# Kernel tuning notes

Hardware: AMD Instinct MI355X
Metric: run time of the kernel (lower is better)

## Reference

```python
import jax, jax.numpy as jnp
import numpy as np

N_NODES = 100000
N_EDGES = 1600000
N_GRAPHS = 1000
D = 128
LATENT = 64
N_LAYERS = 3
EPS = 1e-5


def leaky(z):
    return jnp.where(z >= 0, z, 0.2 * z)


def batchnorm(h, gamma, beta):
    # training-mode BN: biased batch statistics over axis 0
    m = jnp.mean(h, axis=0)
    v = jnp.mean(jnp.square(h - m), axis=0)
    return (h - m) * jax.lax.rsqrt(v + EPS) * gamma + beta


def setup_inputs() -> dict:
    key = jax.random.key(0)
    ks = jax.random.split(key, 8)
    x = jax.random.normal(ks[0], (N_NODES, D), dtype=jnp.float32)
    edge_index = jax.random.randint(ks[1], (2, N_EDGES), 0, N_NODES, dtype=jnp.int32)
    batch = jnp.sort(jax.random.randint(ks[2], (N_NODES,), 0, N_GRAPHS, dtype=jnp.int32))
    s = 1.0 / np.sqrt(D)
    W1 = jax.random.normal(ks[3], (N_LAYERS, D, D), dtype=jnp.float32) * s
    W2 = jax.random.normal(ks[4], (N_LAYERS, D, D), dtype=jnp.float32) * s
    fc_W = jax.random.normal(ks[5], (D, LATENT), dtype=jnp.float32) * s
    return {
        'x': x, 'edge_index': edge_index, 'batch': batch,
        'W1': W1, 'b1': jnp.zeros((N_LAYERS, D), jnp.float32),
        'g1': jnp.ones((N_LAYERS, D), jnp.float32), 'bt1': jnp.zeros((N_LAYERS, D), jnp.float32),
        'W2': W2, 'b2': jnp.zeros((N_LAYERS, D), jnp.float32),
        'bn_g': jnp.ones((D,), jnp.float32), 'bn_b': jnp.zeros((D,), jnp.float32),
        'fc_W': fc_W, 'fc_b': jnp.zeros((LATENT,), jnp.float32),
    }


def reference(x, edge_index, batch, W1, b1, g1, bt1, W2, b2, bn_g, bn_b, fc_W, fc_b):
    src, dst = edge_index[0], edge_index[1]
    n = x.shape[0]
    for l in range(N_LAYERS):
        x_res = x
        # GIN aggregation: (1 + eps) * x + sum_{j in N(i)} x_j, eps = 0
        agg = jax.ops.segment_sum(x[src], dst, num_segments=n) + x
        h = leaky(agg @ W1[l] + b1[l])
        h = batchnorm(h, g1[l], bt1[l])
        h = leaky(h @ W2[l] + b2[l])
        x = h + x_res  # residual (dropout disabled in eval)
    pooled = jax.ops.segment_sum(x, batch, num_segments=N_GRAPHS)  # [G, D]
    out = batchnorm(pooled, bn_g, bn_b)
    return out @ fc_W + fc_b
```

## Files before the change

kernel.cpp:

```cpp
#include <hip/hip_runtime.h>

#define N_NODES 100000
#define N_EDGES 1600000
#define N_GRAPHS 1000
#define D 128
#define LATENT 64
#define EPS 1e-5f
#define NB ((N_NODES + 255) / 256)
#define NBUCK 196
#define BSH 9
#define CONVX_BLOCKS ((N_NODES * D / 4 + 255) / 256)

typedef unsigned short u16;
typedef unsigned int u32;
typedef __attribute__((ext_vector_type(8))) short short8;
typedef __attribute__((ext_vector_type(4))) float f32x4;

__device__ __forceinline__ float bf2f(u32 u) {
    union { u32 i; float f; } c; c.i = u << 16; return c.f;
}
__device__ __forceinline__ u16 f2bf(float f) {
    union { float f; u32 u; } c; c.f = f;
    u32 u = c.u;
    return (u16)((u + 0x7fffu + ((u >> 16) & 1u)) >> 16);
}


__global__ void init_misc(const float* __restrict__ W1, const float* __restrict__ W2,
                          u16* __restrict__ Wt, const float* __restrict__ x,
                          u16* __restrict__ xb, float* __restrict__ colsumAll,
                          int* __restrict__ bhist,
                          int* __restrict__ gs, int* __restrict__ ge) {
    int b = blockIdx.x, t = threadIdx.x;
    if (b < 6) {
        const float* src = (b < 3) ? (W1 + (size_t)b * D * D) : (W2 + (size_t)(b - 3) * D * D);
        u16* dst = Wt + (size_t)b * D * D;
        for (int i = t; i < D * D; i += 256) {
            int k = i >> 7, n = i & 127;
            dst[n * D + k] = f2bf(src[i]);
        }
    } else if (b == 6) {
        for (int i = t; i < 6 * 256; i += 256) colsumAll[i] = 0.f;
        if (t < NBUCK) bhist[t] = 0;
        for (int i = t; i < N_GRAPHS; i += 256) { gs[i] = 0x7fffffff; ge[i] = 0; }
    } else {
        int idx = (b - 7) * 256 + t;
        if (idx < N_NODES * D / 4) {
            float4 v = *(const float4*)&x[(size_t)idx * 4];
            u32 lo = (u32)f2bf(v.x) | ((u32)f2bf(v.y) << 16);
            u32 hi = (u32)f2bf(v.z) | ((u32)f2bf(v.w) << 16);
            *(uint2*)&xb[(size_t)idx * 4] = make_uint2(lo, hi);
        }
    }
}


__global__ void bucket_hist(const int* __restrict__ dst, int* __restrict__ bhist) {
    __shared__ int cnt[256];
    int t = threadIdx.x;
    cnt[t] = 0;
    __syncthreads();
    int base = blockIdx.x * 4096 + t * 16;
#pragma unroll
    for (int i = 0; i < 16; ++i) {
        int e = base + i;
        if (e < N_EDGES) atomicAdd(&cnt[dst[e] >> BSH], 1);
    }
    __syncthreads();
    if (t < NBUCK && cnt[t] > 0) atomicAdd(&bhist[t], cnt[t]);
}

__global__ void bucket_scan(const int* __restrict__ bhist, int* __restrict__ bstart,
                            int* __restrict__ gbcur) {
    __shared__ int s[256];
    int t = threadIdx.x;
    int v = (t < NBUCK) ? bhist[t] : 0;
    s[t] = v;
    __syncthreads();
    for (int off = 1; off < 256; off <<= 1) {
        int a = (t >= off) ? s[t - off] : 0;
        __syncthreads();
        s[t] += a;
        __syncthreads();
    }
    if (t < NBUCK) { int ex = s[t] - v; bstart[t] = ex; gbcur[t] = ex; }
    if (t == NBUCK - 1) bstart[NBUCK] = s[t];
}

__global__ __launch_bounds__(256)
void bucket_scatter(const int* __restrict__ src, const int* __restrict__ dst,
                    int* __restrict__ gbcur, u32* __restrict__ ebp) {
    __shared__ int cnt[256], loff[256], basev[256], scn[256];
    __shared__ u32 pp[4096];
    __shared__ unsigned char pbkt[4096];
    int t = threadIdx.x;
    cnt[t] = 0;
    __syncthreads();
    int ebase = blockIdx.x * 4096;
    int b[16], r[16];
    u32 pk[16];
#pragma unroll
    for (int i = 0; i < 16; ++i) {
        int e = ebase + t * 16 + i;
        bool ok = e < N_EDGES;
        int d = ok ? dst[e] : 0;
        int sv = ok ? src[e] : 0;
        pk[i] = ((u32)sv << BSH) | (u32)(d & 511);
        b[i] = ok ? (d >> BSH) : -1;
    }
#pragma unroll
    for (int i = 0; i < 16; ++i)
        r[i] = (b[i] >= 0) ? atomicAdd(&cnt[b[i]], 1) : 0;
    __syncthreads();
    int c = cnt[t];
    scn[t] = c;
    __syncthreads();
    for (int off = 1; off < 256; off <<= 1) {
        int a = (t >= off) ? scn[t - off] : 0;
        __syncthreads();
        scn[t] += a;
        __syncthreads();
    }
    loff[t] = scn[t] - c;
    if (c > 0) basev[t] = atomicAdd(&gbcur[t], c);
    __syncthreads();
#pragma unroll
    for (int i = 0; i < 16; ++i) {
        if (b[i] >= 0) {
            int p = loff[b[i]] + r[i];
            pp[p] = pk[i];
            pbkt[p] = (unsigned char)b[i];
        }
    }
    __syncthreads();
    int total = min(4096, N_EDGES - ebase);
    for (int i = t; i < total; i += 256) {
        int bb = pbkt[i];
        int g = basev[bb] + (i - loff[bb]);
        ebp[g] = pp[i];
    }
}

__global__ void hist_local(const u32* __restrict__ ebp, const int* __restrict__ bstart,
                           int* __restrict__ deg) {
    __shared__ int h[512];
    int b = blockIdx.x, t = threadIdx.x;
    int nbase = b << BSH;
    h[t] = 0; h[t + 256] = 0;
    __syncthreads();
    int e0 = bstart[b], e1 = bstart[b + 1];
    for (int e = e0 + t; e < e1; e += 256)
        atomicAdd(&h[ebp[e] & 511], 1);
    __syncthreads();
    int nlen = min(512, N_NODES - nbase);
    if (t < nlen) deg[nbase + t] = h[t];
    if (t + 256 < nlen) deg[nbase + t + 256] = h[t + 256];
}

__global__ void scan_block_sum(const int* __restrict__ deg, int* __restrict__ bsum) {
    __shared__ int s[256];
    int t = threadIdx.x;
    int i = blockIdx.x * 256 + t;
    s[t] = (i < N_NODES) ? deg[i] : 0;
    __syncthreads();
    for (int off = 128; off > 0; off >>= 1) {
        if (t < off) s[t] += s[t + off];
        __syncthreads();
    }
    if (t == 0) bsum[blockIdx.x] = s[0];
}

__global__ void scan_top(const int* __restrict__ bsum, int* __restrict__ boff) {
    __shared__ int s[512];
    int t = threadIdx.x;
    int v = (t < NB) ? bsum[t] : 0;
    s[t] = v;
    __syncthreads();
    for (int off = 1; off < 512; off <<= 1) {
        int add = (t >= off) ? s[t - off] : 0;
        __syncthreads();
        s[t] += add;
        __syncthreads();
    }
    if (t < NB) boff[t] = s[t] - v;
}

__global__ void scan_apply(const int* __restrict__ deg, const int* __restrict__ boff,
                           int* __restrict__ offsets) {
    __shared__ int s[256];
    int t = threadIdx.x;
    int i = blockIdx.x * 256 + t;
    int v = (i < N_NODES) ? deg[i] : 0;
    s[t] = v;
    __syncthreads();
    for (int off = 1; off < 256; off <<= 1) {
        int add = (t >= off) ? s[t - off] : 0;
        __syncthreads();
        s[t] += add;
        __syncthreads();
    }
    int base = boff[blockIdx.x];
    if (i < N_NODES) offsets[i] = base + s[t] - v;
    if (i == N_NODES - 1) offsets[N_NODES] = base + s[t];
}

__global__ void csr_fill_local(const u32* __restrict__ ebp, const int* __restrict__ bstart,
                               const int* __restrict__ offsets, int* __restrict__ csr) {
    __shared__ int cur[512];
    int b = blockIdx.x, t = threadIdx.x;
    int nbase = b << BSH;
    int nlen = min(512, N_NODES - nbase);
    if (t < nlen) cur[t] = offsets[nbase + t];
    if (t + 256 < nlen) cur[t + 256] = offsets[nbase + t + 256];
    __syncthreads();
    int e0 = bstart[b], e1 = bstart[b + 1];
    for (int e = e0 + t; e < e1; e += 256) {
        u32 pk = ebp[e];
        int p = atomicAdd(&cur[pk & 511], 1);
        csr[p] = (int)(pk >> BSH);
    }
}


__device__ __forceinline__ void acc8(float* a, uint4 v) {
    a[0] += bf2f(v.x & 0xffff); a[1] += bf2f(v.x >> 16);
    a[2] += bf2f(v.y & 0xffff); a[3] += bf2f(v.y >> 16);
    a[4] += bf2f(v.z & 0xffff); a[5] += bf2f(v.z >> 16);
    a[6] += bf2f(v.w & 0xffff); a[7] += bf2f(v.w >> 16);
}

__global__ void agg_kernel(const u16* __restrict__ xb, const int* __restrict__ csr,
                           const int* __restrict__ offsets, u16* __restrict__ ab) {
    int t = blockIdx.x * blockDim.x + threadIdx.x;
    int node = t >> 4;
    if (node >= N_NODES) return;
    int lane = t & 15;
    const uint4* xp = (const uint4*)(xb + lane * 8);
    float a[8] = {0, 0, 0, 0, 0, 0, 0, 0};
    acc8(a, xp[(size_t)node * 16]);
    int s = offsets[node], e = offsets[node + 1];
    int p = s;
    for (; p + 8 <= e; p += 8) {
        int j0 = csr[p], j1 = csr[p + 1], j2 = csr[p + 2], j3 = csr[p + 3];
        int j4 = csr[p + 4], j5 = csr[p + 5], j6 = csr[p + 6], j7 = csr[p + 7];
        uint4 v0 = xp[(size_t)j0 * 16];
        uint4 v1 = xp[(size_t)j1 * 16];
        uint4 v2 = xp[(size_t)j2 * 16];
        uint4 v3 = xp[(size_t)j3 * 16];
        uint4 v4 = xp[(size_t)j4 * 16];
        uint4 v5 = xp[(size_t)j5 * 16];
        uint4 v6 = xp[(size_t)j6 * 16];
        uint4 v7 = xp[(size_t)j7 * 16];
        acc8(a, v0); acc8(a, v1); acc8(a, v2); acc8(a, v3);
        acc8(a, v4); acc8(a, v5); acc8(a, v6); acc8(a, v7);
    }
    for (; p + 4 <= e; p += 4) {
        int j0 = csr[p], j1 = csr[p + 1], j2 = csr[p + 2], j3 = csr[p + 3];
        uint4 v0 = xp[(size_t)j0 * 16];
        uint4 v1 = xp[(size_t)j1 * 16];
        uint4 v2 = xp[(size_t)j2 * 16];
        uint4 v3 = xp[(size_t)j3 * 16];
        acc8(a, v0); acc8(a, v1); acc8(a, v2); acc8(a, v3);
    }
    for (; p < e; ++p)
        acc8(a, xp[(size_t)csr[p] * 16]);
    uint4 o;
    o.x = (u32)f2bf(a[0]) | ((u32)f2bf(a[1]) << 16);
    o.y = (u32)f2bf(a[2]) | ((u32)f2bf(a[3]) << 16);
    o.z = (u32)f2bf(a[4]) | ((u32)f2bf(a[5]) << 16);
    o.w = (u32)f2bf(a[6]) | ((u32)f2bf(a[7]) << 16);
    *(uint4*)&ab[(size_t)node * D + lane * 8] = o;
}


__global__ __launch_bounds__(256, 4)
void gemm1_mfma(u16* __restrict__ AB, const u16* __restrict__ Wt,
                const float* __restrict__ bias,
                float* __restrict__ colsum, float* __restrict__ colsq) {
    __shared__ u16 As[128 * 128];
    __shared__ float csumL[D], csqL[D];
    int tid = threadIdx.x;
    int row0 = blockIdx.x * 128;

    if (tid < D) { csumL[tid] = 0.f; csqL[tid] = 0.f; }
#pragma unroll
    for (int i = 0; i < 8; ++i) {
        int q = i * 256 + tid;
        int m = q >> 4, kc = q & 15;
        uint4 av = make_uint4(0, 0, 0, 0);
        int gm = row0 + m;
        if (gm < N_NODES) av = *(const uint4*)&AB[(size_t)gm * D + kc * 8];
        *(uint4*)((char*)As + m * 256 + ((kc * 16) ^ ((m & 15) << 4))) = av;
    }
    __syncthreads();

    int lane = tid & 63;
    int wid = tid >> 6;
    int mbase = (wid >> 1) * 64, nbase = (wid & 1) * 64;
    int lr = lane & 15, kg = lane >> 4;
    f32x4 acc[4][4];
#pragma unroll
    for (int mt = 0; mt < 4; ++mt)
#pragma unroll
        for (int nt = 0; nt < 4; ++nt) acc[mt][nt] = (f32x4)0.0f;

    const char* Ap = (const char*)As;
#pragma unroll
    for (int ks = 0; ks < 4; ++ks) {
        int kb2 = ks * 64 + kg * 16;
        short8 af[4], bfr[4];
#pragma unroll
        for (int t = 0; t < 4; ++t) {
            int m = mbase + t * 16 + lr;
            af[t] = *(const short8*)(Ap + m * 256 + (kb2 ^ ((m & 15) << 4)));
            int n = nbase + t * 16 + lr;
            bfr[t] = *(const short8*)&Wt[n * D + ks * 32 + kg * 8];
        }
#pragma unroll
        for (int mt = 0; mt < 4; ++mt)
#pragma unroll
            for (int nt = 0; nt < 4; ++nt)
                acc[mt][nt] = __builtin_amdgcn_mfma_f32_16x16x32_bf16(af[mt], bfr[nt], acc[mt][nt], 0, 0, 0);
    }

    float bv[4], ls[4] = {0, 0, 0, 0}, lq[4] = {0, 0, 0, 0};
#pragma unroll
    for (int nt = 0; nt < 4; ++nt) bv[nt] = bias[nbase + nt * 16 + lr];
#pragma unroll
    for (int mt = 0; mt < 4; ++mt) {
#pragma unroll
        for (int r = 0; r < 4; ++r) {
            int gm = row0 + mbase + mt * 16 + kg * 4 + r;
            if (gm < N_NODES) {
#pragma unroll
                for (int nt = 0; nt < 4; ++nt) {
                    float z = acc[mt][nt][r] + bv[nt];
                    z = (z >= 0.f) ? z : 0.2f * z;
                    AB[(size_t)gm * D + nbase + nt * 16 + lr] = f2bf(z);
                    ls[nt] += z; lq[nt] += z * z;
                }
            }
        }
    }
#pragma unroll
    for (int nt = 0; nt < 4; ++nt) {
        ls[nt] += __shfl_down(ls[nt], 32); ls[nt] += __shfl_down(ls[nt], 16);
        lq[nt] += __shfl_down(lq[nt], 32); lq[nt] += __shfl_down(lq[nt], 16);
    }
    if (lane < 16) {
#pragma unroll
        for (int nt = 0; nt < 4; ++nt) {
            atomicAdd(&csumL[nbase + nt * 16 + lane], ls[nt]);
            atomicAdd(&csqL[nbase + nt * 16 + lane], lq[nt]);
        }
    }
    __syncthreads();
    if (tid < D) {
        atomicAdd(&colsum[tid], csumL[tid]);
        atomicAdd(&colsq[tid], csqL[tid]);
    }
}

__global__ __launch_bounds__(256, 4)
void gemm2_mfma(const u16* __restrict__ HB, const u16* __restrict__ Wt,
                const float* __restrict__ bias,
                const float* __restrict__ colsum, const float* __restrict__ colsq,
                const float* __restrict__ gamma, const float* __restrict__ beta,
                const u16* __restrict__ xres, u16* __restrict__ xbout) {
    __shared__ u16 As[128 * 128];
    __shared__ float scL[D], shL[D];
    int tid = threadIdx.x;
    int row0 = blockIdx.x * 128;

    if (tid < D) {
        float m = colsum[tid] * (1.0f / N_NODES);
        float var = fmaxf(colsq[tid] * (1.0f / N_NODES) - m * m, 0.f);
        float sc = gamma[tid] * rsqrtf(var + EPS);
        scL[tid] = sc;
        shL[tid] = beta[tid] - m * sc;
    }
    __syncthreads();

#pragma unroll
    for (int i = 0; i < 8; ++i) {
        int q = i * 256 + tid;
        int m = q >> 4, kc = q & 15;
        uint4 av = make_uint4(0, 0, 0, 0);
        int gm = row0 + m;
        if (gm < N_NODES) {
            uint4 h = *(const uint4*)&HB[(size_t)gm * D + kc * 8];
            float4 s0 = *(const float4*)&scL[kc * 8];
            float4 s1 = *(const float4*)&scL[kc * 8 + 4];
            float4 t0 = *(const float4*)&shL[kc * 8];
            float4 t1 = *(const float4*)&shL[kc * 8 + 4];
            float f0 = bf2f(h.x & 0xffff) * s0.x + t0.x;
            float f1 = bf2f(h.x >> 16)    * s0.y + t0.y;
            float f2 = bf2f(h.y & 0xffff) * s0.z + t0.z;
            float f3 = bf2f(h.y >> 16)    * s0.w + t0.w;
            float f4 = bf2f(h.z & 0xffff) * s1.x + t1.x;
            float f5 = bf2f(h.z >> 16)    * s1.y + t1.y;
            float f6 = bf2f(h.w & 0xffff) * s1.z + t1.z;
            float f7 = bf2f(h.w >> 16)    * s1.w + t1.w;
            av.x = (u32)f2bf(f0) | ((u32)f2bf(f1) << 16);
            av.y = (u32)f2bf(f2) | ((u32)f2bf(f3) << 16);
            av.z = (u32)f2bf(f4) | ((u32)f2bf(f5) << 16);
            av.w = (u32)f2bf(f6) | ((u32)f2bf(f7) << 16);
        }
        *(uint4*)((char*)As + m * 256 + ((kc * 16) ^ ((m & 15) << 4))) = av;
    }
    __syncthreads();

    int lane = tid & 63;
    int wid = tid >> 6;
    int mbase = (wid >> 1) * 64, nbase = (wid & 1) * 64;
    int lr = lane & 15, kg = lane >> 4;
    f32x4 acc[4][4];
#pragma unroll
    for (int mt = 0; mt < 4; ++mt)
#pragma unroll
        for (int nt = 0; nt < 4; ++nt) acc[mt][nt] = (f32x4)0.0f;

    const char* Ap = (const char*)As;
#pragma unroll
    for (int ks = 0; ks < 4; ++ks) {
        int kb2 = ks * 64 + kg * 16;
        short8 af[4], bfr[4];
#pragma unroll
        for (int t = 0; t < 4; ++t) {
            int m = mbase + t * 16 + lr;
            af[t] = *(const short8*)(Ap + m * 256 + (kb2 ^ ((m & 15) << 4)));
            int n = nbase + t * 16 + lr;
            bfr[t] = *(const short8*)&Wt[n * D + ks * 32 + kg * 8];
        }
#pragma unroll
        for (int mt = 0; mt < 4; ++mt)
#pragma unroll
            for (int nt = 0; nt < 4; ++nt)
                acc[mt][nt] = __builtin_amdgcn_mfma_f32_16x16x32_bf16(af[mt], bfr[nt], acc[mt][nt], 0, 0, 0);
    }

    float bv[4];
#pragma unroll
    for (int nt = 0; nt < 4; ++nt) bv[nt] = bias[nbase + nt * 16 + lr];
#pragma unroll
    for (int mt = 0; mt < 4; ++mt) {
#pragma unroll
        for (int r = 0; r < 4; ++r) {
            int gm = row0 + mbase + mt * 16 + kg * 4 + r;
            if (gm < N_NODES) {
#pragma unroll
                for (int nt = 0; nt < 4; ++nt) {
                    int gn = nbase + nt * 16 + lr;
                    float z = acc[mt][nt][r] + bv[nt];
                    z = (z >= 0.f) ? z : 0.2f * z;
                    float o = z + bf2f((u32)xres[(size_t)gm * D + gn]);
                    xbout[(size_t)gm * D + gn] = f2bf(o);
                }
            }
        }
    }
}


__global__ void bounds_kernel(const int* __restrict__ batch, int* __restrict__ gs, int* __restrict__ ge) {
    int i = blockIdx.x * blockDim.x + threadIdx.x;
    if (i >= N_NODES) return;
    int b = batch[i];
    if (i == 0) {
        gs[b] = 0;
    } else {
        int bp = batch[i - 1];
        if (bp != b) { gs[b] = i; ge[bp] = i; }
    }
    if (i == N_NODES - 1) ge[b] = N_NODES;
}

__global__ void pool_kernel(const u16* __restrict__ xb, const int* __restrict__ gs,
                            const int* __restrict__ ge, float* __restrict__ pooled) {
    int g = blockIdx.x, f = threadIdx.x;
    int s = gs[g], e = ge[g];
    float a0 = 0.f, a1 = 0.f, a2 = 0.f, a3 = 0.f;
    int i = s;
    for (; i + 4 <= e; i += 4) {
        a0 += bf2f((u32)xb[(size_t)i * D + f]);
        a1 += bf2f((u32)xb[(size_t)(i + 1) * D + f]);
        a2 += bf2f((u32)xb[(size_t)(i + 2) * D + f]);
        a3 += bf2f((u32)xb[(size_t)(i + 3) * D + f]);
    }
    for (; i < e; ++i) a0 += bf2f((u32)xb[(size_t)i * D + f]);
    pooled[g * D + f] = (a0 + a1) + (a2 + a3);
}

__global__ void pooled_bn(const float* __restrict__ pooled, const float* __restrict__ g,
                          const float* __restrict__ b, float* __restrict__ pscale,
                          float* __restrict__ pshift) {
    int c = blockIdx.x;
    int t = threadIdx.x;
    float s = 0.f, q = 0.f;
    for (int gi = t; gi < N_GRAPHS; gi += 256) {
        float v = pooled[gi * D + c];
        s += v; q += v * v;
    }
#pragma unroll
    for (int off = 32; off > 0; off >>= 1) {
        s += __shfl_down(s, off);
        q += __shfl_down(q, off);
    }
    __shared__ float ss[4], qq[4];
    int lane = t & 63, w = t >> 6;
    if (lane == 0) { ss[w] = s; qq[w] = q; }
    __syncthreads();
    if (t == 0) {
        float S = (ss[0] + ss[1]) + (ss[2] + ss[3]);
        float Q = (qq[0] + qq[1]) + (qq[2] + qq[3]);
        float m = S / N_GRAPHS;
        float var = fmaxf(Q / N_GRAPHS - m * m, 0.f);
        float sc = g[c] * rsqrtf(var + EPS);
        pscale[c] = sc;
        pshift[c] = b[c] - m * sc;
    }
}

__global__ void out_kernel(const float* __restrict__ pooled, const float* __restrict__ pscale,
                           const float* __restrict__ pshift, const float* __restrict__ fcW,
                           const float* __restrict__ fcb, float* __restrict__ out) {
    int idx = blockIdx.x * blockDim.x + threadIdx.x;
    if (idx >= N_GRAPHS * LATENT) return;
    int g = idx >> 6, j = idx & 63;
    float acc = fcb[j];
    for (int c = 0; c < D; ++c) {
        float pv = pooled[g * D + c] * pscale[c] + pshift[c];
        acc += pv * fcW[c * LATENT + j];
    }
    out[idx] = acc;
}


extern "C" void kernel_launch(void* const* d_in, const int* in_sizes, int n_in,
                              void* d_out, int out_size, void* d_ws, size_t ws_size,
                              hipStream_t stream) {
    const float* x_in = (const float*)d_in[0];
    const int* edges  = (const int*)d_in[1];
    const int* batch  = (const int*)d_in[2];
    const float* W1   = (const float*)d_in[3];
    const float* b1   = (const float*)d_in[4];
    const float* g1   = (const float*)d_in[5];
    const float* bt1  = (const float*)d_in[6];
    const float* W2   = (const float*)d_in[7];
    const float* b2   = (const float*)d_in[8];
    const float* bng  = (const float*)d_in[9];
    const float* bnb  = (const float*)d_in[10];
    const float* fcW  = (const float*)d_in[11];
    const float* fcb  = (const float*)d_in[12];
    float* out = (float*)d_out;
    const int* srcp = edges;
    const int* dstp = edges + N_EDGES;

    char* p = (char*)d_ws;
    auto alloc = [&](size_t bytes) -> char* {
        char* r = p;
        p += (bytes + 511) & ~(size_t)511;
        return r;
    };
    u16*   XB      = (u16*)alloc((size_t)N_NODES * D * 2);
    u16*   AB      = (u16*)alloc((size_t)N_NODES * D * 2);
    int*   csr     = (int*)alloc((size_t)N_EDGES * 4);
    u32*   ebp     = (u32*)alloc((size_t)N_EDGES * 4);
    int*   deg     = (int*)alloc((size_t)N_NODES * 4);
    int*   offsets = (int*)alloc((size_t)(N_NODES + 1) * 4);
    int*   bsum    = (int*)alloc((size_t)NB * 4);
    int*   boff    = (int*)alloc((size_t)NB * 4);
    int*   bhist   = (int*)alloc((size_t)NBUCK * 4);
    int*   bstart  = (int*)alloc((size_t)(NBUCK + 1) * 4);
    int*   gbcur   = (int*)alloc((size_t)NBUCK * 4);
    u16*   Wtb     = (u16*)alloc((size_t)6 * D * D * 2);
    float* colsumA = (float*)alloc((size_t)6 * 256 * 4);
    int*   gs      = (int*)alloc(N_GRAPHS * 4);
    int*   ge      = (int*)alloc(N_GRAPHS * 4);
    float* pooled  = (float*)alloc((size_t)N_GRAPHS * D * 4);
    float* pscale  = (float*)alloc(D * 4);
    float* pshift  = (float*)alloc(D * 4);

    init_misc<<<7 + CONVX_BLOCKS, 256, 0, stream>>>(W1, W2, Wtb, x_in, XB, colsumA,
                                                    bhist, gs, ge);

    const int EGRID = (N_EDGES + 4095) / 4096;
    bucket_hist<<<EGRID, 256, 0, stream>>>(dstp, bhist);
    bucket_scan<<<1, 256, 0, stream>>>(bhist, bstart, gbcur);
    bucket_scatter<<<EGRID, 256, 0, stream>>>(srcp, dstp, gbcur, ebp);
    hist_local<<<NBUCK, 256, 0, stream>>>(ebp, bstart, deg);
    scan_block_sum<<<NB, 256, 0, stream>>>(deg, bsum);
    scan_top<<<1, 512, 0, stream>>>(bsum, boff);
    scan_apply<<<NB, 256, 0, stream>>>(deg, boff, offsets);
    csr_fill_local<<<NBUCK, 256, 0, stream>>>(ebp, bstart, offsets, csr);

    const int GEMM_GRID = (N_NODES + 127) / 128;
    const int AGG_GRID = (N_NODES * 16 + 255) / 256;
    for (int l = 0; l < 3; ++l) {
        agg_kernel<<<AGG_GRID, 256, 0, stream>>>(XB, csr, offsets, AB);
        gemm1_mfma<<<GEMM_GRID, 256, 0, stream>>>(AB, Wtb + (size_t)l * D * D, b1 + l * D,
                                                  colsumA + l * 256, colsumA + l * 256 + 128);
        gemm2_mfma<<<GEMM_GRID, 256, 0, stream>>>(AB, Wtb + (size_t)(3 + l) * D * D, b2 + l * D,
                                                  colsumA + l * 256, colsumA + l * 256 + 128,
                                                  g1 + l * D, bt1 + l * D, XB, XB);
    }

    bounds_kernel<<<NB, 256, 0, stream>>>(batch, gs, ge);
    pool_kernel<<<N_GRAPHS, D, 0, stream>>>(XB, gs, ge, pooled);
    pooled_bn<<<D, 256, 0, stream>>>(pooled, bng, bnb, pscale, pshift);
    out_kernel<<<(N_GRAPHS * LATENT + 255) / 256, 256, 0, stream>>>(pooled, pscale, pshift,
                                                                    fcW, fcb, out);
}
```

Baseline: 467.1 us.

## Fuse neighbor aggregation into first GEMM via shared-memory staging

The separate gather-sum aggregation kernel is merged into the first MFMA GEMM kernel. Each 128-row block now gathers its nodes' neighbor sums straight into the swizzled LDS tile, so the aggregated matrix is no longer written to global memory and read back, and one launch per layer goes away. The cost is that the gather now runs inside a GEMM kernel held to a 256-thread block with LDS-limited occupancy (782 blocks), processing 16 nodes per pass over 8 serial passes. That may hide less of the random-gather latency than the old standalone kernel with many small blocks.

```diff
diff --git a/kernel.cpp b/kernel.cpp
--- a/kernel.cpp
+++ b/kernel.cpp
@@ -229,68 +229,61 @@
     a[6] += bf2f(v.w & 0xffff); a[7] += bf2f(v.w >> 16);
 }
 
-__global__ void agg_kernel(const u16* __restrict__ xb, const int* __restrict__ csr,
-                           const int* __restrict__ offsets, u16* __restrict__ ab) {
-    int t = blockIdx.x * blockDim.x + threadIdx.x;
-    int node = t >> 4;
-    if (node >= N_NODES) return;
-    int lane = t & 15;
-    const uint4* xp = (const uint4*)(xb + lane * 8);
-    float a[8] = {0, 0, 0, 0, 0, 0, 0, 0};
-    acc8(a, xp[(size_t)node * 16]);
-    int s = offsets[node], e = offsets[node + 1];
-    int p = s;
-    for (; p + 8 <= e; p += 8) {
-        int j0 = csr[p], j1 = csr[p + 1], j2 = csr[p + 2], j3 = csr[p + 3];
-        int j4 = csr[p + 4], j5 = csr[p + 5], j6 = csr[p + 6], j7 = csr[p + 7];
-        uint4 v0 = xp[(size_t)j0 * 16];
-        uint4 v1 = xp[(size_t)j1 * 16];
-        uint4 v2 = xp[(size_t)j2 * 16];
-        uint4 v3 = xp[(size_t)j3 * 16];
-        uint4 v4 = xp[(size_t)j4 * 16];
-        uint4 v5 = xp[(size_t)j5 * 16];
-        uint4 v6 = xp[(size_t)j6 * 16];
-        uint4 v7 = xp[(size_t)j7 * 16];
-        acc8(a, v0); acc8(a, v1); acc8(a, v2); acc8(a, v3);
-        acc8(a, v4); acc8(a, v5); acc8(a, v6); acc8(a, v7);
-    }
-    for (; p + 4 <= e; p += 4) {
-        int j0 = csr[p], j1 = csr[p + 1], j2 = csr[p + 2], j3 = csr[p + 3];
-        uint4 v0 = xp[(size_t)j0 * 16];
-        uint4 v1 = xp[(size_t)j1 * 16];
-        uint4 v2 = xp[(size_t)j2 * 16];
-        uint4 v3 = xp[(size_t)j3 * 16];
-        acc8(a, v0); acc8(a, v1); acc8(a, v2); acc8(a, v3);
-    }
-    for (; p < e; ++p)
-        acc8(a, xp[(size_t)csr[p] * 16]);
-    uint4 o;
-    o.x = (u32)f2bf(a[0]) | ((u32)f2bf(a[1]) << 16);
-    o.y = (u32)f2bf(a[2]) | ((u32)f2bf(a[3]) << 16);
-    o.z = (u32)f2bf(a[4]) | ((u32)f2bf(a[5]) << 16);
-    o.w = (u32)f2bf(a[6]) | ((u32)f2bf(a[7]) << 16);
-    *(uint4*)&ab[(size_t)node * D + lane * 8] = o;
-}
-
-
 __global__ __launch_bounds__(256, 4)
-void gemm1_mfma(u16* __restrict__ AB, const u16* __restrict__ Wt,
-                const float* __restrict__ bias,
-                float* __restrict__ colsum, float* __restrict__ colsq) {
+void agg_gemm1_mfma(const u16* __restrict__ xb, const int* __restrict__ csr,
+                    const int* __restrict__ offsets,
+                    const u16* __restrict__ Wt, const float* __restrict__ bias,
+                    u16* __restrict__ HB,
+                    float* __restrict__ colsum, float* __restrict__ colsq) {
     __shared__ u16 As[128 * 128];
     __shared__ float csumL[D], csqL[D];
     int tid = threadIdx.x;
     int row0 = blockIdx.x * 128;
 
     if (tid < D) { csumL[tid] = 0.f; csqL[tid] = 0.f; }
-#pragma unroll
-    for (int i = 0; i < 8; ++i) {
-        int q = i * 256 + tid;
-        int m = q >> 4, kc = q & 15;
-        uint4 av = make_uint4(0, 0, 0, 0);
-        int gm = row0 + m;
-        if (gm < N_NODES) av = *(const uint4*)&AB[(size_t)gm * D + kc * 8];
-        *(uint4*)((char*)As + m * 256 + ((kc * 16) ^ ((m & 15) << 4))) = av;
+
+    int lane16 = tid & 15;
+    const uint4* xp = (const uint4*)xb + lane16;
+#pragma unroll 1
+    for (int pass = 0; pass < 8; ++pass) {
+        int m = pass * 16 + (tid >> 4);
+        int node = row0 + m;
+        float a[8] = {0, 0, 0, 0, 0, 0, 0, 0};
+        if (node < N_NODES) {
+            acc8(a, xp[(size_t)node * 16]);
+            int s = offsets[node], e = offsets[node + 1];
+            int p = s;
+            for (; p + 8 <= e; p += 8) {
+                int j0 = csr[p], j1 = csr[p + 1], j2 = csr[p + 2], j3 = csr[p + 3];
+                int j4 = csr[p + 4], j5 = csr[p + 5], j6 = csr[p + 6], j7 = csr[p + 7];
+                uint4 v0 = xp[(size_t)j0 * 16];
+                uint4 v1 = xp[(size_t)j1 * 16];
+                uint4 v2 = xp[(size_t)j2 * 16];
+                uint4 v3 = xp[(size_t)j3 * 16];
+                uint4 v4 = xp[(size_t)j4 * 16];
+                uint4 v5 = xp[(size_t)j5 * 16];
+                uint4 v6 = xp[(size_t)j6 * 16];
+                uint4 v7 = xp[(size_t)j7 * 16];
+                acc8(a, v0); acc8(a, v1); acc8(a, v2); acc8(a, v3);
+                acc8(a, v4); acc8(a, v5); acc8(a, v6); acc8(a, v7);
+            }
+            for (; p + 4 <= e; p += 4) {
+                int j0 = csr[p], j1 = csr[p + 1], j2 = csr[p + 2], j3 = csr[p + 3];
+                uint4 v0 = xp[(size_t)j0 * 16];
+                uint4 v1 = xp[(size_t)j1 * 16];
+                uint4 v2 = xp[(size_t)j2 * 16];
+                uint4 v3 = xp[(size_t)j3 * 16];
+                acc8(a, v0); acc8(a, v1); acc8(a, v2); acc8(a, v3);
+            }
+            for (; p < e; ++p)
+                acc8(a, xp[(size_t)csr[p] * 16]);
+        }
+        uint4 o;
+        o.x = (u32)f2bf(a[0]) | ((u32)f2bf(a[1]) << 16);
+        o.y = (u32)f2bf(a[2]) | ((u32)f2bf(a[3]) << 16);
+        o.z = (u32)f2bf(a[4]) | ((u32)f2bf(a[5]) << 16);
+        o.w = (u32)f2bf(a[6]) | ((u32)f2bf(a[7]) << 16);
+        *(uint4*)((char*)As + m * 256 + ((lane16 * 16) ^ ((m & 15) << 4))) = o;
     }
     __syncthreads();
 
@@ -336,7 +329,7 @@
                 for (int nt = 0; nt < 4; ++nt) {
                     float z = acc[mt][nt][r] + bv[nt];
                     z = (z >= 0.f) ? z : 0.2f * z;
-                    AB[(size_t)gm * D + nbase + nt * 16 + lr] = f2bf(z);
+                    HB[(size_t)gm * D + nbase + nt * 16 + lr] = f2bf(z);
                     ls[nt] += z; lq[nt] += z * z;
                 }
             }
@@ -563,7 +556,7 @@
         return r;
     };
     u16*   XB      = (u16*)alloc((size_t)N_NODES * D * 2);
-    u16*   AB      = (u16*)alloc((size_t)N_NODES * D * 2);
+    u16*   HB      = (u16*)alloc((size_t)N_NODES * D * 2);
     int*   csr     = (int*)alloc((size_t)N_EDGES * 4);
     u32*   ebp     = (u32*)alloc((size_t)N_EDGES * 4);
     int*   deg     = (int*)alloc((size_t)N_NODES * 4);
@@ -595,12 +588,11 @@
     csr_fill_local<<<NBUCK, 256, 0, stream>>>(ebp, bstart, offsets, csr);
 
     const int GEMM_GRID = (N_NODES + 127) / 128;
-    const int AGG_GRID = (N_NODES * 16 + 255) / 256;
     for (int l = 0; l < 3; ++l) {
-        agg_kernel<<<AGG_GRID, 256, 0, stream>>>(XB, csr, offsets, AB);
-        gemm1_mfma<<<GEMM_GRID, 256, 0, stream>>>(AB, Wtb + (size_t)l * D * D, b1 + l * D,
-                                                  colsumA + l * 256, colsumA + l * 256 + 128);
-        gemm2_mfma<<<GEMM_GRID, 256, 0, stream>>>(AB, Wtb + (size_t)(3 + l) * D * D, b2 + l * D,
+        agg_gemm1_mfma<<<GEMM_GRID, 256, 0, stream>>>(XB, csr, offsets,
+                                                      Wtb + (size_t)l * D * D, b1 + l * D, HB,
+                                                      colsumA + l * 256, colsumA + l * 256 + 128);
+        gemm2_mfma<<<GEMM_GRID, 256, 0, stream>>>(HB, Wtb + (size_t)(3 + l) * D * D, b2 + l * D,
                                                   colsumA + l * 256, colsumA + l * 256 + 128,
                                                   g1 + l * D, bt1 + l * D, XB, XB);
     }
```

New measurement: 434.4 us. 1.08x faster.
